# Kernel tuning notes

Measured on AMD Instinct MI355X. Metric: run time of the kernel, lower is better.

The kernel has to match this reference:

```python
import jax, jax.numpy as jnp
import numpy as np
import math

D_MODEL = 1024
N_HEAD = 16


def setup_inputs() -> dict:
    key = jax.random.key(0)
    k1, k2, k3 = jax.random.split(key, 3)
    B, S, E = 2, 2048, D_MODEL
    x = jax.random.normal(k1, (B, S, E), dtype=jnp.float32)
    # Linear weights stored as (in, out); init scaled like typical transformer init
    w_attn = jax.random.normal(k2, (E, 3 * E), dtype=jnp.float32) * (1.0 / math.sqrt(E))
    w_proj = jax.random.normal(k3, (E, E), dtype=jnp.float32) * (1.0 / math.sqrt(E))
    return {"x": x, "w_attn": w_attn, "w_proj": w_proj}


def reference(x, w_attn, w_proj):
    B, S, E = x.shape
    H = N_HEAD
    Dh = E // H
    qkv = x @ w_attn  # (B, S, 3E)
    q, k, v = jnp.split(qkv, 3, axis=-1)
    # (B, H, S, Dh)
    q = q.reshape(B, S, H, Dh).transpose(0, 2, 1, 3)
    k = k.reshape(B, S, H, Dh).transpose(0, 2, 1, 3)
    v = v.reshape(B, S, H, Dh).transpose(0, 2, 1, 3)
    scale = 1.0 / math.sqrt(Dh)
    att = jnp.einsum('bhqd,bhkd->bhqk', q, k) * scale  # (B, H, S, S)
    causal = jnp.tril(jnp.ones((S, S), dtype=bool))
    att = jnp.where(causal, att, -jnp.inf)
    att = jax.nn.softmax(att, axis=-1)
    # dropout = 0.0 (eval mode) -> identity
    y = jnp.einsum('bhqk,bhkd->bhqd', att, v)  # (B, H, S, Dh)
    y = y.transpose(0, 2, 1, 3).reshape(B, S, E)
    return y @ w_proj
```

## Files before the change

kernel.cpp:

```cpp
#include <hip/hip_runtime.h>
#include <hip/hip_bf16.h>

#define S_LEN 2048
#define EMB   1024
#define NH    16
#define DH    64
#define QKV_LD 3072

typedef __attribute__((ext_vector_type(8)))  __bf16 bf16x8;
typedef __attribute__((ext_vector_type(4)))  __bf16 bf16x4;
typedef __attribute__((ext_vector_type(4)))  float  f32x4;
typedef __attribute__((ext_vector_type(16))) float  f32x16;
typedef __attribute__((ext_vector_type(2)))  unsigned int u32x2;

__device__ __forceinline__ void gl_lds16(const void* g, void* l) {
  __builtin_amdgcn_global_load_lds(
      (const __attribute__((address_space(1))) void*)g,
      (__attribute__((address_space(3))) void*)l,
      16, 0, 0);
}

__global__ __launch_bounds__(256)
void prep_fused(const float* __restrict__ x, __bf16* __restrict__ xb,
                const float* __restrict__ w_attn, __bf16* __restrict__ wat,
                const float* __restrict__ w_proj, __bf16* __restrict__ wpt,
                int n8) {
  __shared__ float T[64][65];
  const int bid = blockIdx.x;
  const int tid = threadIdx.x;

  if (bid < 2048) {
    int i = bid * 256 + tid;
    if (i >= n8) return;
    const f32x4* p = (const f32x4*)(x + (size_t)i * 8);
    f32x4 a = p[0], b = p[1];
    bf16x8 o;
    #pragma unroll
    for (int j = 0; j < 4; j++) { o[j] = (__bf16)a[j]; o[4 + j] = (__bf16)b[j]; }
    *(bf16x8*)(xb + (size_t)i * 8) = o;
    return;
  }

  const float* W; __bf16* Wt; int K, N, k0, n0;
  if (bid < 2048 + 768) {
    int t = bid - 2048;
    W = w_attn; Wt = wat; K = 1024; N = 3072;
    n0 = (t % 48) * 64; k0 = (t / 48) * 64;
  } else {
    int t = bid - 2816;
    W = w_proj; Wt = wpt; K = 1024; N = 1024;
    n0 = (t & 15) * 64; k0 = (t >> 4) * 64;
  }
  #pragma unroll
  for (int t = 0; t < 16; t++) {
    int idx = tid + t * 256;
    int r = idx >> 6, c = idx & 63;
    T[r][c] = W[(size_t)(k0 + r) * N + n0 + c];
  }
  __syncthreads();
  #pragma unroll
  for (int t = 0; t < 16; t++) {
    int idx = tid + t * 256;
    int r = idx >> 6, c = idx & 63;
    Wt[(size_t)(n0 + r) * K + k0 + c] = (__bf16)T[c][r];
  }
}

#define TM 128
#define TK 32

template <typename OutT, int TNv>
__global__ __launch_bounds__(256, 2)
void gemm_bf16_mfma(const __bf16* __restrict__ A, const __bf16* __restrict__ Bt,
                    OutT* __restrict__ C, int M, int N, int K) {
  __shared__ __align__(16) __bf16 As[2][TM][TK];
  __shared__ __align__(16) __bf16 Bs[2][TNv][TK];
  const int tid  = threadIdx.x;
  const int lane = tid & 63;
  const int w    = tid >> 6;
  const int wr   = w >> 1, wc = w & 1;
  const int brow = blockIdx.y * TM;
  const int bcol = blockIdx.x * TNv;
  const int l15  = lane & 15;
  const int grp  = lane >> 4;

  constexpr int NBI = TNv / 64;
  constexpr int WCT = TNv / 2;
  constexpr int NN  = WCT / 16;

  auto stage = [&](int k0, int buf) {
    #pragma unroll
    for (int j = 0; j < 2; j++) {
      const int cid = w * 128 + j * 64 + lane;
      const int row = cid >> 2, k8 = (cid & 3) * 8;
      gl_lds16(A + (size_t)(brow + row) * K + k0 + k8,
               &As[buf][0][0] + (size_t)(w * 128 + j * 64) * 8);
    }
    #pragma unroll
    for (int j = 0; j < NBI; j++) {
      const int cid = (w * NBI + j) * 64 + lane;
      const int row = cid >> 2, k8 = (cid & 3) * 8;
      gl_lds16(Bt + (size_t)(bcol + row) * K + k0 + k8,
               &Bs[buf][0][0] + (size_t)((w * NBI + j) * 64) * 8);
    }
  };

  f32x4 acc[4][NN];
  #pragma unroll
  for (int m = 0; m < 4; m++)
    #pragma unroll
    for (int n = 0; n < NN; n++) acc[m][n] = (f32x4){0.f, 0.f, 0.f, 0.f};

  stage(0, 0);
  __syncthreads();

  const int nk = K / TK;
  for (int kt = 0; kt < nk; kt++) {
    const int cur = kt & 1;
    if (kt + 1 < nk) stage((kt + 1) * TK, cur ^ 1);

    bf16x8 a[4], b[NN];
    #pragma unroll
    for (int m = 0; m < 4; m++)
      a[m] = *(const bf16x8*)&As[cur][wr * 64 + m * 16 + l15][grp * 8];
    #pragma unroll
    for (int n = 0; n < NN; n++)
      b[n] = *(const bf16x8*)&Bs[cur][wc * WCT + n * 16 + l15][grp * 8];
    #pragma unroll
    for (int m = 0; m < 4; m++)
      #pragma unroll
      for (int n = 0; n < NN; n++)
        acc[m][n] = __builtin_amdgcn_mfma_f32_16x16x32_bf16(a[m], b[n], acc[m][n], 0, 0, 0);

    __syncthreads();
  }

  #pragma unroll
  for (int m = 0; m < 4; m++)
    #pragma unroll
    for (int r = 0; r < 4; r++) {
      const size_t row = (size_t)(brow + wr * 64 + m * 16 + grp * 4 + r);
      #pragma unroll
      for (int n = 0; n < NN; n++)
        C[row * N + bcol + wc * WCT + n * 16 + l15] = (OutT)acc[m][n][r];
    }
}

#define QB 64
#define KB 64
#define QSCALE 0.18033688f

__global__ __launch_bounds__(256, 4)
void attn_mfma(const __bf16* __restrict__ qkv, __bf16* __restrict__ y) {
  __shared__ __align__(16) __bf16 Ks[2][KB][64];
  __shared__ __align__(16) __bf16 Vs[2][4096];

  const int tid  = threadIdx.x;
  const int lane = tid & 63;
  const int w    = tid >> 6;

  const int bid = blockIdx.x;
  const int swz = (bid & 7) * 128 + (bid >> 3);
  const int g   = swz >> 5;
  const int i   = swz & 31;
  const int zig = (i & 1) ? (i >> 1) : 31 - (i >> 1);
  const int qtile = (g & 1) ? 31 - zig : zig;
  const int h = g & 15, b = g >> 4;

  const __bf16* base = qkv + (size_t)b * S_LEN * QKV_LD;

  const int l31 = lane & 31;
  const int hl  = lane >> 5;
  const int qh  = w >> 1;
  const int kh  = w & 1;

  const int voff32 = ((lane >> 4) & 1) * 2048 + hl * 128 + (lane & 15) * 8
                   + kh * 1024;

  auto stageK = [&](int j0, int buf) {
    #pragma unroll
    for (int j = 0; j < 2; j++) {
      const int cid = w * 128 + j * 64 + lane;
      const int r = cid >> 3, pc = cid & 7;
      const int lc = pc ^ (r & 7);
      gl_lds16(base + (size_t)(j0 + r) * QKV_LD + EMB + h * DH + lc * 8,
               (char*)&Ks[buf][0][0] + (w * 128 + j * 64) * 16);
    }
  };
  auto stageV = [&](int j0, int buf) {
    #pragma unroll
    for (int j = 0; j < 2; j++) {
      const int cid = w * 128 + j * 64 + lane;
      const int db = cid >> 7, sk = (cid >> 3) & 15;
      const int jr = (cid >> 1) & 3, ch = cid & 1;
      gl_lds16(base + (size_t)(j0 + sk * 4 + jr) * QKV_LD + 2 * EMB + h * DH
                    + db * 16 + ch * 8,
               (char*)&Vs[buf][0] + (w * 128 + j * 64) * 16);
    }
  };

  const int qbase = qtile * QB;
  const int ntiles = qtile + 1;
  const int q = qbase + qh * 32 + l31;

  bf16x8 qf[4];
  {
    const __bf16* qp = base + (size_t)q * QKV_LD + h * DH;
    #pragma unroll
    for (int dq = 0; dq < 4; dq++) {
      bf16x8 v = *(const bf16x8*)(qp + dq * 16 + hl * 8);
      #pragma unroll
      for (int i2 = 0; i2 < 8; i2++) qf[dq][i2] = (__bf16)((float)v[i2] * QSCALE);
    }
  }

  f32x16 o_acc[2];
  #pragma unroll
  for (int d2 = 0; d2 < 2; d2++)
    #pragma unroll
    for (int r = 0; r < 16; r++) o_acc[d2][r] = 0.f;
  float m = -1e30f, l = 0.f;

  auto process = [&](int cur, int j0, bool masked) {
    f32x16 s;
    #pragma unroll
    for (int r = 0; r < 16; r++) s[r] = 0.f;
    const int krow = kh * 32 + l31;
    __builtin_amdgcn_s_setprio(1);
    #pragma unroll
    for (int dq = 0; dq < 4; dq++) {
      bf16x8 kf = *(const bf16x8*)&Ks[cur][krow][((dq * 2 + hl) ^ (krow & 7)) * 8];
      s = __builtin_amdgcn_mfma_f32_32x32x16_bf16(kf, qf[dq], s, 0, 0, 0);
    }
    __builtin_amdgcn_s_setprio(0);

    if (masked) {
      const int lim = q - j0 - kh * 32 - 4 * hl;
      #pragma unroll
      for (int r = 0; r < 16; r++) {
        const int kl = (r & 3) + 8 * (r >> 2);
        if (kl > lim) s[r] = -2e30f;
      }
    }

    float tmax = s[0];
    #pragma unroll
    for (int r = 1; r < 16; r++) tmax = fmaxf(tmax, s[r]);
    tmax = fmaxf(tmax, __shfl_xor(tmax, 32));

    const bool grow = !__all(tmax <= m + 8.0f);
    float corr = 1.f;
    if (grow) {
      const float mnew = fmaxf(m, tmax);
      corr = __builtin_amdgcn_exp2f(m - mnew);
      m = mnew;
    }

    const unsigned vb =
        (unsigned)(uintptr_t)(__attribute__((address_space(3))) char*)(&Vs[cur][0])
        + (unsigned)voff32;
    u32x2 tv[8];
    asm volatile("ds_read_b64_tr_b16 %0, %1 offset:0"    : "=v"(tv[0]) : "v"(vb));
    asm volatile("ds_read_b64_tr_b16 %0, %1 offset:256"  : "=v"(tv[1]) : "v"(vb));
    asm volatile("ds_read_b64_tr_b16 %0, %1 offset:512"  : "=v"(tv[2]) : "v"(vb));
    asm volatile("ds_read_b64_tr_b16 %0, %1 offset:768"  : "=v"(tv[3]) : "v"(vb));
    asm volatile("ds_read_b64_tr_b16 %0, %1 offset:4096" : "=v"(tv[4]) : "v"(vb));
    asm volatile("ds_read_b64_tr_b16 %0, %1 offset:4352" : "=v"(tv[5]) : "v"(vb));
    asm volatile("ds_read_b64_tr_b16 %0, %1 offset:4608" : "=v"(tv[6]) : "v"(vb));
    asm volatile("ds_read_b64_tr_b16 %0, %1 offset:4864" : "=v"(tv[7]) : "v"(vb));

    float psum = 0.f;
    #pragma unroll
    for (int r = 0; r < 16; r++) {
      float p = __builtin_amdgcn_exp2f(s[r] - m);
      s[r] = p;
      psum += p;
    }

    bf16x8 pb0, pb1;
    #pragma unroll
    for (int i2 = 0; i2 < 8; i2++) {
      pb0[i2] = (__bf16)s[i2];
      pb1[i2] = (__bf16)s[8 + i2];
    }

    if (grow) {
      #pragma unroll
      for (int d2 = 0; d2 < 2; d2++)
        #pragma unroll
        for (int r = 0; r < 16; r++) o_acc[d2][r] *= corr;
    }

    asm volatile("s_waitcnt lgkmcnt(0)");
    __builtin_amdgcn_sched_barrier(0);
    __builtin_amdgcn_s_setprio(1);
    #pragma unroll
    for (int d2 = 0; d2 < 2; d2++) {
      bf16x8 a0, a1;
      ((u32x2*)&a0)[0] = tv[d2 * 4 + 0]; ((u32x2*)&a0)[1] = tv[d2 * 4 + 1];
      ((u32x2*)&a1)[0] = tv[d2 * 4 + 2]; ((u32x2*)&a1)[1] = tv[d2 * 4 + 3];
      o_acc[d2] = __builtin_amdgcn_mfma_f32_32x32x16_bf16(a0, pb0, o_acc[d2], 0, 0, 0);
      o_acc[d2] = __builtin_amdgcn_mfma_f32_32x32x16_bf16(a1, pb1, o_acc[d2], 0, 0, 0);
    }
    __builtin_amdgcn_s_setprio(0);

    psum += __shfl_xor(psum, 32);
    l = grow ? (l * corr + psum) : (l + psum);
  };

  stageK(0, 0);
  stageV(0, 0);
  __syncthreads();

  #pragma unroll 1
  for (int kt = 0; kt < ntiles - 1; kt++) {
    const int cur = kt & 1;
    stageK((kt + 1) * KB, cur ^ 1);
    stageV((kt + 1) * KB, cur ^ 1);
    process(cur, kt * KB, false);
    __syncthreads();
  }

  process((ntiles - 1) & 1, (ntiles - 1) * KB, true);

  __syncthreads();
  float* exO  = (float*)&Vs[0][0];
  float* exML = (float*)&Ks[0][0][0];
  const int slot = qh * 64 + lane;
  if (kh) {
    #pragma unroll
    for (int r = 0; r < 16; r++) {
      exO[r * 128 + slot]        = o_acc[0][r];
      exO[(16 + r) * 128 + slot] = o_acc[1][r];
    }
    exML[slot]       = m;
    exML[128 + slot] = l;
  }
  __syncthreads();
  if (!kh) {
    const float m1  = exML[slot];
    const float l1v = exML[128 + slot];
    const float mm = fmaxf(m, m1);
    const float c0 = __builtin_amdgcn_exp2f(m - mm);
    const float c1 = __builtin_amdgcn_exp2f(m1 - mm);
    const float inv = 1.f / (l * c0 + l1v * c1);
    __bf16* yrow = y + ((size_t)(b * S_LEN + q)) * EMB + h * DH;
    #pragma unroll
    for (int d2 = 0; d2 < 2; d2++)
      #pragma unroll
      for (int rq = 0; rq < 4; rq++) {
        bf16x4 o4;
        #pragma unroll
        for (int j = 0; j < 4; j++) {
          const int r = rq * 4 + j;
          float v = (o_acc[d2][r] * c0 + exO[(d2 * 16 + r) * 128 + slot] * c1) * inv;
          o4[j] = (__bf16)v;
        }
        *(bf16x4*)&yrow[d2 * 32 + rq * 8 + hl * 4] = o4;
      }
  }
}

extern "C" void kernel_launch(void* const* d_in, const int* in_sizes, int n_in,
                              void* d_out, int out_size, void* d_ws, size_t ws_size,
                              hipStream_t stream) {
  const float* x      = (const float*)d_in[0];
  const float* w_attn = (const float*)d_in[1];
  const float* w_proj = (const float*)d_in[2];
  float* out = (float*)d_out;

  const int B = in_sizes[0] / (S_LEN * EMB);
  const int M = B * S_LEN;

  __bf16* xb   = (__bf16*)d_ws;
  __bf16* wat  = xb  + (size_t)M * EMB;
  __bf16* wpt  = wat + (size_t)QKV_LD * EMB;
  __bf16* qkvb = wpt + (size_t)EMB * EMB;
  __bf16* yb   = qkvb + (size_t)M * QKV_LD;

  {
    int n8 = (M * EMB) / 8;
    prep_fused<<<dim3(3072), 256, 0, stream>>>(x, xb, w_attn, wat, w_proj, wpt, n8);
  }

  dim3 g1(QKV_LD / 128, M / TM);
  gemm_bf16_mfma<__bf16, 128><<<g1, 256, 0, stream>>>(xb, wat, qkvb, M, QKV_LD, EMB);

  attn_mfma<<<dim3(32 * NH * B), 256, 0, stream>>>(qkvb, yb);

  dim3 g3(EMB / 64, M / TM);
  gemm_bf16_mfma<float, 64><<<g3, 256, 0, stream>>>(yb, wpt, out, M, EMB, EMB);
}
```

Measured before the change: 109.2 us.

## Split long causal attention rows across two blocks with a merge kernel

Causal attention work is rebalanced so that query tiles 16-31, which have the most key tiles, are split into two halves along the key dimension, each handled by its own block. The halves write unnormalized partial outputs plus max/sum statistics into scratch memory, reusing the output buffer and the weight workspace. A new merge kernel combines them into the bf16 result. The goal is more uniform per-block work and better load balance across the XCDs, at the cost of an extra launch and extra fp32 scratch traffic; the occupancy hint is also raised from 4 to 5 blocks.

```diff
diff --git a/kernel.cpp b/kernel.cpp
--- a/kernel.cpp
+++ b/kernel.cpp
@@ -150,8 +150,9 @@
 #define KB 64
 #define QSCALE 0.18033688f
 
-__global__ __launch_bounds__(256, 4)
-void attn_mfma(const __bf16* __restrict__ qkv, __bf16* __restrict__ y) {
+__global__ __launch_bounds__(256, 5)
+void attn_mfma(const __bf16* __restrict__ qkv, __bf16* __restrict__ y,
+               float* __restrict__ pO, float* __restrict__ pml) {
   __shared__ __align__(16) __bf16 Ks[2][KB][64];
   __shared__ __align__(16) __bf16 Vs[2][4096];
 
@@ -160,12 +161,26 @@
   const int w    = tid >> 6;
 
   const int bid = blockIdx.x;
-  const int swz = (bid & 7) * 128 + (bid >> 3);
-  const int g   = swz >> 5;
-  const int i   = swz & 31;
-  const int zig = (i & 1) ? (i >> 1) : 31 - (i >> 1);
-  const int qtile = (g & 1) ? 31 - zig : zig;
+  const int xcd = bid & 7;
+  const int j   = bid >> 3;
+  const int g   = xcd * 4 + j / 48;
+  const int idx = j % 48;
+  const int t3  = idx / 3, r3 = idx - t3 * 3;
+
+  int qtile, it0, it1, khalf;
+  bool split, diag;
+  if (r3 == 2) {
+    qtile = 15 - t3; split = false; khalf = 0;
+    it0 = 0; it1 = qtile + 1; diag = true;
+  } else {
+    qtile = 31 - t3; split = true; khalf = r3;
+    const int half = (qtile + 2) >> 1;
+    it0 = khalf ? half : 0;
+    it1 = khalf ? qtile + 1 : half;
+    diag = (khalf == 1);
+  }
   const int h = g & 15, b = g >> 4;
+  const int pidx = split ? ((g * 16 + (qtile - 16)) * 2 + khalf) : 0;
 
   const __bf16* base = qkv + (size_t)b * S_LEN * QKV_LD;
 
@@ -179,28 +194,27 @@
 
   auto stageK = [&](int j0, int buf) {
     #pragma unroll
-    for (int j = 0; j < 2; j++) {
-      const int cid = w * 128 + j * 64 + lane;
+    for (int jj = 0; jj < 2; jj++) {
+      const int cid = w * 128 + jj * 64 + lane;
       const int r = cid >> 3, pc = cid & 7;
       const int lc = pc ^ (r & 7);
       gl_lds16(base + (size_t)(j0 + r) * QKV_LD + EMB + h * DH + lc * 8,
-               (char*)&Ks[buf][0][0] + (w * 128 + j * 64) * 16);
+               (char*)&Ks[buf][0][0] + (w * 128 + jj * 64) * 16);
     }
   };
   auto stageV = [&](int j0, int buf) {
     #pragma unroll
-    for (int j = 0; j < 2; j++) {
-      const int cid = w * 128 + j * 64 + lane;
+    for (int jj = 0; jj < 2; jj++) {
+      const int cid = w * 128 + jj * 64 + lane;
       const int db = cid >> 7, sk = (cid >> 3) & 15;
       const int jr = (cid >> 1) & 3, ch = cid & 1;
       gl_lds16(base + (size_t)(j0 + sk * 4 + jr) * QKV_LD + 2 * EMB + h * DH
                     + db * 16 + ch * 8,
-               (char*)&Vs[buf][0] + (w * 128 + j * 64) * 16);
+               (char*)&Vs[buf][0] + (w * 128 + jj * 64) * 16);
     }
   };
 
   const int qbase = qtile * QB;
-  const int ntiles = qtile + 1;
   const int q = qbase + qh * 32 + l31;
 
   bf16x8 qf[4];
@@ -308,20 +322,21 @@
     l = grow ? (l * corr + psum) : (l + psum);
   };
 
-  stageK(0, 0);
-  stageV(0, 0);
+  stageK(it0 * KB, 0);
+  stageV(it0 * KB, 0);
   __syncthreads();
 
+  const int nt = it1 - it0;
   #pragma unroll 1
-  for (int kt = 0; kt < ntiles - 1; kt++) {
-    const int cur = kt & 1;
-    stageK((kt + 1) * KB, cur ^ 1);
-    stageV((kt + 1) * KB, cur ^ 1);
-    process(cur, kt * KB, false);
+  for (int tt = 0; tt < nt - 1; tt++) {
+    const int cur = tt & 1;
+    stageK((it0 + tt + 1) * KB, cur ^ 1);
+    stageV((it0 + tt + 1) * KB, cur ^ 1);
+    process(cur, (it0 + tt) * KB, false);
     __syncthreads();
   }
 
-  process((ntiles - 1) & 1, (ntiles - 1) * KB, true);
+  process((nt - 1) & 1, (it1 - 1) * KB, diag);
 
   __syncthreads();
   float* exO  = (float*)&Vs[0][0];
@@ -343,21 +358,77 @@
     const float mm = fmaxf(m, m1);
     const float c0 = __builtin_amdgcn_exp2f(m - mm);
     const float c1 = __builtin_amdgcn_exp2f(m1 - mm);
-    const float inv = 1.f / (l * c0 + l1v * c1);
-    __bf16* yrow = y + ((size_t)(b * S_LEN + q)) * EMB + h * DH;
-    #pragma unroll
-    for (int d2 = 0; d2 < 2; d2++)
-      #pragma unroll
-      for (int rq = 0; rq < 4; rq++) {
-        bf16x4 o4;
+    const float lsum = l * c0 + l1v * c1;
+    if (split) {
+      float* prow = pO + (size_t)pidx * 4096 + (size_t)(qh * 32 + l31) * 64;
+      #pragma unroll
+      for (int d2 = 0; d2 < 2; d2++)
         #pragma unroll
-        for (int j = 0; j < 4; j++) {
-          const int r = rq * 4 + j;
-          float v = (o_acc[d2][r] * c0 + exO[(d2 * 16 + r) * 128 + slot] * c1) * inv;
-          o4[j] = (__bf16)v;
+        for (int rq = 0; rq < 4; rq++) {
+          f32x4 o4;
+          #pragma unroll
+          for (int jj = 0; jj < 4; jj++) {
+            const int r = rq * 4 + jj;
+            o4[jj] = o_acc[d2][r] * c0 + exO[(d2 * 16 + r) * 128 + slot] * c1;
+          }
+          *(f32x4*)&prow[d2 * 32 + rq * 8 + hl * 4] = o4;
         }
-        *(bf16x4*)&yrow[d2 * 32 + rq * 8 + hl * 4] = o4;
+      if (!hl) {
+        pml[(size_t)pidx * 128 + qh * 32 + l31]      = mm;
+        pml[(size_t)pidx * 128 + 64 + qh * 32 + l31] = lsum;
       }
+    } else {
+      const float inv = 1.f / lsum;
+      __bf16* yrow = y + ((size_t)(b * S_LEN + q)) * EMB + h * DH;
+      #pragma unroll
+      for (int d2 = 0; d2 < 2; d2++)
+        #pragma unroll
+        for (int rq = 0; rq < 4; rq++) {
+          bf16x4 o4;
+          #pragma unroll
+          for (int jj = 0; jj < 4; jj++) {
+            const int r = rq * 4 + jj;
+            float v = (o_acc[d2][r] * c0 + exO[(d2 * 16 + r) * 128 + slot] * c1) * inv;
+            o4[jj] = (__bf16)v;
+          }
+          *(bf16x4*)&yrow[d2 * 32 + rq * 8 + hl * 4] = o4;
+        }
+    }
+  }
+}
+
+__global__ __launch_bounds__(256)
+void attn_merge(const float* __restrict__ pO, const float* __restrict__ pml,
+                __bf16* __restrict__ y) {
+  const int mid = blockIdx.x;
+  const int g = mid >> 4, qrel = mid & 15;
+  const int qt = 16 + qrel;
+  const int b = g >> 4, h = g & 15;
+  const int p0 = (g * 16 + qrel) * 2, p1 = p0 + 1;
+  const int row = threadIdx.x >> 2;
+  const int d0  = (threadIdx.x & 3) * 16;
+
+  const float mA = pml[(size_t)p0 * 128 + row];
+  const float lA = pml[(size_t)p0 * 128 + 64 + row];
+  const float mB = pml[(size_t)p1 * 128 + row];
+  const float lB = pml[(size_t)p1 * 128 + 64 + row];
+  const float mm = fmaxf(mA, mB);
+  const float cA = __builtin_amdgcn_exp2f(mA - mm);
+  const float cB = __builtin_amdgcn_exp2f(mB - mm);
+  const float inv = 1.f / (lA * cA + lB * cB);
+
+  const float* OA = pO + (size_t)p0 * 4096 + (size_t)row * 64 + d0;
+  const float* OB = pO + (size_t)p1 * 4096 + (size_t)row * 64 + d0;
+  __bf16* yr = y + ((size_t)(b * S_LEN + qt * 64 + row)) * EMB + h * DH + d0;
+  #pragma unroll
+  for (int i = 0; i < 4; i++) {
+    f32x4 va = *(const f32x4*)(OA + i * 4);
+    f32x4 vb = *(const f32x4*)(OB + i * 4);
+    bf16x4 o;
+    #pragma unroll
+    for (int jj = 0; jj < 4; jj++)
+      o[jj] = (__bf16)((va[jj] * cA + vb[jj] * cB) * inv);
+    *(bf16x4*)(yr + i * 4) = o;
   }
 }
 
@@ -378,6 +449,9 @@
   __bf16* qkvb = wpt + (size_t)EMB * EMB;
   __bf16* yb   = qkvb + (size_t)M * QKV_LD;
 
+  float* pO  = out;
+  float* pml = (float*)wat;
+
   {
     int n8 = (M * EMB) / 8;
     prep_fused<<<dim3(3072), 256, 0, stream>>>(x, xb, w_attn, wat, w_proj, wpt, n8);
@@ -386,7 +460,8 @@
   dim3 g1(QKV_LD / 128, M / TM);
   gemm_bf16_mfma<__bf16, 128><<<g1, 256, 0, stream>>>(xb, wat, qkvb, M, QKV_LD, EMB);
 
-  attn_mfma<<<dim3(32 * NH * B), 256, 0, stream>>>(qkvb, yb);
+  attn_mfma<<<dim3(1536), 256, 0, stream>>>(qkvb, yb, pO, pml);
+  attn_merge<<<dim3(512), 256, 0, stream>>>(pO, pml, yb);
 
   dim3 g3(EMB / 64, M / TM);
   gemm_bf16_mfma<float, 64><<<g3, 256, 0, stream>>>(yb, wpt, out, M, EMB, EMB);
```

New measurement: 147.0 us. 34.6% more time.

## Use 128-key tiles with single-buffered LDS and in-iteration staged prefetch

Applied to the files above, without the earlier changes.

Doubles the key tile to 128 so each wave does two QK^T and four PV MFMAs per iteration, halving loop iterations and barrier overhead. Drops LDS double-buffering for a single 32KB buffer, and issues the next K and V loads mid-iteration once the current reads have drained, guarded by extra barriers. The last tile is always masked. Register pressure rises (two score blocks, 16 V fragments), and the single buffer exposes load latency at the top of each iteration.

```diff
diff --git a/kernel.cpp b/kernel.cpp
--- a/kernel.cpp
+++ b/kernel.cpp
@@ -147,13 +147,12 @@
 }
 
 #define QB 64
-#define KB 64
+#define KB 128
 #define QSCALE 0.18033688f
 
 __global__ __launch_bounds__(256, 4)
 void attn_mfma(const __bf16* __restrict__ qkv, __bf16* __restrict__ y) {
-  __shared__ __align__(16) __bf16 Ks[2][KB][64];
-  __shared__ __align__(16) __bf16 Vs[2][4096];
+  __shared__ __align__(16) char SMEM[33792];
 
   const int tid  = threadIdx.x;
   const int lane = tid & 63;
@@ -174,33 +173,33 @@
   const int qh  = w >> 1;
   const int kh  = w & 1;
 
-  const int voff32 = ((lane >> 4) & 1) * 2048 + hl * 128 + (lane & 15) * 8
-                   + kh * 1024;
-
-  auto stageK = [&](int j0, int buf) {
-    #pragma unroll
-    for (int j = 0; j < 2; j++) {
-      const int cid = w * 128 + j * 64 + lane;
+  const int voff32 = ((lane >> 4) & 1) * 2048 + hl * 128 + (lane & 15) * 8;
+
+  auto stageK = [&](int j0) {
+    #pragma unroll
+    for (int jj = 0; jj < 4; jj++) {
+      const int cid = w * 256 + jj * 64 + lane;
       const int r = cid >> 3, pc = cid & 7;
       const int lc = pc ^ (r & 7);
       gl_lds16(base + (size_t)(j0 + r) * QKV_LD + EMB + h * DH + lc * 8,
-               (char*)&Ks[buf][0][0] + (w * 128 + j * 64) * 16);
+               SMEM + cid * 16);
     }
   };
-  auto stageV = [&](int j0, int buf) {
-    #pragma unroll
-    for (int j = 0; j < 2; j++) {
-      const int cid = w * 128 + j * 64 + lane;
-      const int db = cid >> 7, sk = (cid >> 3) & 15;
-      const int jr = (cid >> 1) & 3, ch = cid & 1;
-      gl_lds16(base + (size_t)(j0 + sk * 4 + jr) * QKV_LD + 2 * EMB + h * DH
-                    + db * 16 + ch * 8,
-               (char*)&Vs[buf][0] + (w * 128 + j * 64) * 16);
+  auto stageV = [&](int j0) {
+    #pragma unroll
+    for (int jj = 0; jj < 4; jj++) {
+      const int cid = w * 256 + jj * 64 + lane;
+      const int c  = cid >> 9;
+      const int cc = cid & 511;
+      const int db = cc >> 7, sk = (cc >> 3) & 15;
+      const int jr = (cc >> 1) & 3, ch = cc & 1;
+      gl_lds16(base + (size_t)(j0 + c * 64 + sk * 4 + jr) * QKV_LD + 2 * EMB
+                    + h * DH + db * 16 + ch * 8,
+               SMEM + 16384 + cid * 16);
     }
   };
 
   const int qbase = qtile * QB;
-  const int ntiles = qtile + 1;
   const int q = qbase + qh * 32 + l31;
 
   bf16x8 qf[4];
@@ -221,31 +220,70 @@
     for (int r = 0; r < 16; r++) o_acc[d2][r] = 0.f;
   float m = -1e30f, l = 0.f;
 
-  auto process = [&](int cur, int j0, bool masked) {
-    f32x16 s;
-    #pragma unroll
-    for (int r = 0; r < 16; r++) s[r] = 0.f;
-    const int krow = kh * 32 + l31;
+  const int krow0 = kh * 64 + l31;
+  const int ksw   = l31 & 7;
+
+  auto iter = [&](int j0, bool masked, int jn, bool do_stage) {
+    asm volatile("s_waitcnt vmcnt(0)" ::: "memory");
+    __builtin_amdgcn_s_barrier();
+    __builtin_amdgcn_sched_barrier(0);
+
+    f32x16 s0, s1;
+    #pragma unroll
+    for (int r = 0; r < 16; r++) { s0[r] = 0.f; s1[r] = 0.f; }
     __builtin_amdgcn_s_setprio(1);
     #pragma unroll
     for (int dq = 0; dq < 4; dq++) {
-      bf16x8 kf = *(const bf16x8*)&Ks[cur][krow][((dq * 2 + hl) ^ (krow & 7)) * 8];
-      s = __builtin_amdgcn_mfma_f32_32x32x16_bf16(kf, qf[dq], s, 0, 0, 0);
+      const int col = ((dq * 2 + hl) ^ ksw) * 16;
+      bf16x8 kf0 = *(const bf16x8*)(SMEM + krow0 * 128 + col);
+      bf16x8 kf1 = *(const bf16x8*)(SMEM + (krow0 + 32) * 128 + col);
+      s0 = __builtin_amdgcn_mfma_f32_32x32x16_bf16(kf0, qf[dq], s0, 0, 0, 0);
+      s1 = __builtin_amdgcn_mfma_f32_32x32x16_bf16(kf1, qf[dq], s1, 0, 0, 0);
     }
     __builtin_amdgcn_s_setprio(0);
 
     if (masked) {
-      const int lim = q - j0 - kh * 32 - 4 * hl;
+      const int lim0 = q - j0 - kh * 64 - 4 * hl;
       #pragma unroll
       for (int r = 0; r < 16; r++) {
         const int kl = (r & 3) + 8 * (r >> 2);
-        if (kl > lim) s[r] = -2e30f;
+        if (kl > lim0)      s0[r] = -2e30f;
+        if (kl > lim0 - 32) s1[r] = -2e30f;
       }
     }
 
-    float tmax = s[0];
-    #pragma unroll
-    for (int r = 1; r < 16; r++) tmax = fmaxf(tmax, s[r]);
+    const unsigned vb =
+        (unsigned)(uintptr_t)(__attribute__((address_space(3))) char*)
+            (SMEM + 16384) + (unsigned)(kh * 8192 + voff32);
+    u32x2 tv0[8], tv1[8];
+    asm volatile("ds_read_b64_tr_b16 %0, %1 offset:0"    : "=v"(tv0[0]) : "v"(vb));
+    asm volatile("ds_read_b64_tr_b16 %0, %1 offset:256"  : "=v"(tv0[1]) : "v"(vb));
+    asm volatile("ds_read_b64_tr_b16 %0, %1 offset:512"  : "=v"(tv0[2]) : "v"(vb));
+    asm volatile("ds_read_b64_tr_b16 %0, %1 offset:768"  : "=v"(tv0[3]) : "v"(vb));
+    asm volatile("ds_read_b64_tr_b16 %0, %1 offset:4096" : "=v"(tv0[4]) : "v"(vb));
+    asm volatile("ds_read_b64_tr_b16 %0, %1 offset:4352" : "=v"(tv0[5]) : "v"(vb));
+    asm volatile("ds_read_b64_tr_b16 %0, %1 offset:4608" : "=v"(tv0[6]) : "v"(vb));
+    asm volatile("ds_read_b64_tr_b16 %0, %1 offset:4864" : "=v"(tv0[7]) : "v"(vb));
+    asm volatile("ds_read_b64_tr_b16 %0, %1 offset:1024" : "=v"(tv1[0]) : "v"(vb));
+    asm volatile("ds_read_b64_tr_b16 %0, %1 offset:1280" : "=v"(tv1[1]) : "v"(vb));
+    asm volatile("ds_read_b64_tr_b16 %0, %1 offset:1536" : "=v"(tv1[2]) : "v"(vb));
+    asm volatile("ds_read_b64_tr_b16 %0, %1 offset:1792" : "=v"(tv1[3]) : "v"(vb));
+    asm volatile("ds_read_b64_tr_b16 %0, %1 offset:5120" : "=v"(tv1[4]) : "v"(vb));
+    asm volatile("ds_read_b64_tr_b16 %0, %1 offset:5376" : "=v"(tv1[5]) : "v"(vb));
+    asm volatile("ds_read_b64_tr_b16 %0, %1 offset:5632" : "=v"(tv1[6]) : "v"(vb));
+    asm volatile("ds_read_b64_tr_b16 %0, %1 offset:5888" : "=v"(tv1[7]) : "v"(vb));
+
+    float x0 = fmaxf(fmaxf(s0[0], s1[0]),  fmaxf(s0[8],  s1[8]));
+    float x1 = fmaxf(fmaxf(s0[1], s1[1]),  fmaxf(s0[9],  s1[9]));
+    float x2 = fmaxf(fmaxf(s0[2], s1[2]),  fmaxf(s0[10], s1[10]));
+    float x3 = fmaxf(fmaxf(s0[3], s1[3]),  fmaxf(s0[11], s1[11]));
+    float x4 = fmaxf(fmaxf(s0[4], s1[4]),  fmaxf(s0[12], s1[12]));
+    float x5 = fmaxf(fmaxf(s0[5], s1[5]),  fmaxf(s0[13], s1[13]));
+    float x6 = fmaxf(fmaxf(s0[6], s1[6]),  fmaxf(s0[14], s1[14]));
+    float x7 = fmaxf(fmaxf(s0[7], s1[7]),  fmaxf(s0[15], s1[15]));
+    x0 = fmaxf(x0, x4); x1 = fmaxf(x1, x5);
+    x2 = fmaxf(x2, x6); x3 = fmaxf(x3, x7);
+    float tmax = fmaxf(fmaxf(x0, x2), fmaxf(x1, x3));
     tmax = fmaxf(tmax, __shfl_xor(tmax, 32));
 
     const bool grow = !__all(tmax <= m + 8.0f);
@@ -256,33 +294,41 @@
       m = mnew;
     }
 
-    const unsigned vb =
-        (unsigned)(uintptr_t)(__attribute__((address_space(3))) char*)(&Vs[cur][0])
-        + (unsigned)voff32;
-    u32x2 tv[8];
-    asm volatile("ds_read_b64_tr_b16 %0, %1 offset:0"    : "=v"(tv[0]) : "v"(vb));
-    asm volatile("ds_read_b64_tr_b16 %0, %1 offset:256"  : "=v"(tv[1]) : "v"(vb));
-    asm volatile("ds_read_b64_tr_b16 %0, %1 offset:512"  : "=v"(tv[2]) : "v"(vb));
-    asm volatile("ds_read_b64_tr_b16 %0, %1 offset:768"  : "=v"(tv[3]) : "v"(vb));
-    asm volatile("ds_read_b64_tr_b16 %0, %1 offset:4096" : "=v"(tv[4]) : "v"(vb));
-    asm volatile("ds_read_b64_tr_b16 %0, %1 offset:4352" : "=v"(tv[5]) : "v"(vb));
-    asm volatile("ds_read_b64_tr_b16 %0, %1 offset:4608" : "=v"(tv[6]) : "v"(vb));
-    asm volatile("ds_read_b64_tr_b16 %0, %1 offset:4864" : "=v"(tv[7]) : "v"(vb));
-
-    float psum = 0.f;
-    #pragma unroll
-    for (int r = 0; r < 16; r++) {
-      float p = __builtin_amdgcn_exp2f(s[r] - m);
-      s[r] = p;
-      psum += p;
-    }
-
-    bf16x8 pb0, pb1;
-    #pragma unroll
-    for (int i2 = 0; i2 < 8; i2++) {
-      pb0[i2] = (__bf16)s[i2];
-      pb1[i2] = (__bf16)s[8 + i2];
-    }
+    __builtin_amdgcn_s_barrier();
+    if (do_stage) stageK(jn);
+
+    asm volatile("s_waitcnt lgkmcnt(0)" ::: "memory");
+    __builtin_amdgcn_sched_barrier(0);
+    __builtin_amdgcn_s_barrier();
+    if (do_stage) stageV(jn);
+
+    float ps0 = 0.f, ps1 = 0.f, ps2 = 0.f, ps3 = 0.f;
+    bf16x8 pb00, pb01, pb10, pb11;
+    #pragma unroll
+    for (int r = 0; r < 16; r += 4) {
+      float p0 = __builtin_amdgcn_exp2f(s0[r]     - m);
+      float p1 = __builtin_amdgcn_exp2f(s0[r + 1] - m);
+      float p2 = __builtin_amdgcn_exp2f(s0[r + 2] - m);
+      float p3 = __builtin_amdgcn_exp2f(s0[r + 3] - m);
+      ps0 += p0; ps1 += p1; ps2 += p2; ps3 += p3;
+      if (r < 8) { pb00[r] = (__bf16)p0; pb00[r+1] = (__bf16)p1;
+                   pb00[r+2] = (__bf16)p2; pb00[r+3] = (__bf16)p3; }
+      else       { pb01[r-8] = (__bf16)p0; pb01[r-7] = (__bf16)p1;
+                   pb01[r-6] = (__bf16)p2; pb01[r-5] = (__bf16)p3; }
+    }
+    #pragma unroll
+    for (int r = 0; r < 16; r += 4) {
+      float p0 = __builtin_amdgcn_exp2f(s1[r]     - m);
+      float p1 = __builtin_amdgcn_exp2f(s1[r + 1] - m);
+      float p2 = __builtin_amdgcn_exp2f(s1[r + 2] - m);
+      float p3 = __builtin_amdgcn_exp2f(s1[r + 3] - m);
+      ps0 += p0; ps1 += p1; ps2 += p2; ps3 += p3;
+      if (r < 8) { pb10[r] = (__bf16)p0; pb10[r+1] = (__bf16)p1;
+                   pb10[r+2] = (__bf16)p2; pb10[r+3] = (__bf16)p3; }
+      else       { pb11[r-8] = (__bf16)p0; pb11[r-7] = (__bf16)p1;
+                   pb11[r-6] = (__bf16)p2; pb11[r-5] = (__bf16)p3; }
+    }
+    float psum = (ps0 + ps1) + (ps2 + ps3);
 
     if (grow) {
       #pragma unroll
@@ -291,16 +337,18 @@
         for (int r = 0; r < 16; r++) o_acc[d2][r] *= corr;
     }
 
-    asm volatile("s_waitcnt lgkmcnt(0)");
-    __builtin_amdgcn_sched_barrier(0);
     __builtin_amdgcn_s_setprio(1);
     #pragma unroll
     for (int d2 = 0; d2 < 2; d2++) {
-      bf16x8 a0, a1;
-      ((u32x2*)&a0)[0] = tv[d2 * 4 + 0]; ((u32x2*)&a0)[1] = tv[d2 * 4 + 1];
-      ((u32x2*)&a1)[0] = tv[d2 * 4 + 2]; ((u32x2*)&a1)[1] = tv[d2 * 4 + 3];
-      o_acc[d2] = __builtin_amdgcn_mfma_f32_32x32x16_bf16(a0, pb0, o_acc[d2], 0, 0, 0);
-      o_acc[d2] = __builtin_amdgcn_mfma_f32_32x32x16_bf16(a1, pb1, o_acc[d2], 0, 0, 0);
+      bf16x8 a0, a1, a2, a3;
+      ((u32x2*)&a0)[0] = tv0[d2 * 4 + 0]; ((u32x2*)&a0)[1] = tv0[d2 * 4 + 1];
+      ((u32x2*)&a1)[0] = tv0[d2 * 4 + 2]; ((u32x2*)&a1)[1] = tv0[d2 * 4 + 3];
+      ((u32x2*)&a2)[0] = tv1[d2 * 4 + 0]; ((u32x2*)&a2)[1] = tv1[d2 * 4 + 1];
+      ((u32x2*)&a3)[0] = tv1[d2 * 4 + 2]; ((u32x2*)&a3)[1] = tv1[d2 * 4 + 3];
+      o_acc[d2] = __builtin_amdgcn_mfma_f32_32x32x16_bf16(a0, pb00, o_acc[d2], 0, 0, 0);
+      o_acc[d2] = __builtin_amdgcn_mfma_f32_32x32x16_bf16(a1, pb01, o_acc[d2], 0, 0, 0);
+      o_acc[d2] = __builtin_amdgcn_mfma_f32_32x32x16_bf16(a2, pb10, o_acc[d2], 0, 0, 0);
+      o_acc[d2] = __builtin_amdgcn_mfma_f32_32x32x16_bf16(a3, pb11, o_acc[d2], 0, 0, 0);
     }
     __builtin_amdgcn_s_setprio(0);
 
@@ -308,24 +356,18 @@
     l = grow ? (l * corr + psum) : (l + psum);
   };
 
-  stageK(0, 0);
-  stageV(0, 0);
+  stageK(0);
+  stageV(0);
+
+  const int nt = (qtile + 2) >> 1;
+  #pragma unroll 1
+  for (int tt = 0; tt < nt; tt++) {
+    iter(tt * KB, tt == nt - 1, (tt + 1) * KB, tt + 1 < nt);
+  }
+
   __syncthreads();
-
-  #pragma unroll 1
-  for (int kt = 0; kt < ntiles - 1; kt++) {
-    const int cur = kt & 1;
-    stageK((kt + 1) * KB, cur ^ 1);
-    stageV((kt + 1) * KB, cur ^ 1);
-    process(cur, kt * KB, false);
-    __syncthreads();
-  }
-
-  process((ntiles - 1) & 1, (ntiles - 1) * KB, true);
-
-  __syncthreads();
-  float* exO  = (float*)&Vs[0][0];
-  float* exML = (float*)&Ks[0][0][0];
+  float* exO  = (float*)SMEM;
+  float* exML = (float*)(SMEM + 32768);
   const int slot = qh * 64 + lane;
   if (kh) {
     #pragma unroll
@@ -351,10 +393,10 @@
       for (int rq = 0; rq < 4; rq++) {
         bf16x4 o4;
         #pragma unroll
-        for (int j = 0; j < 4; j++) {
-          const int r = rq * 4 + j;
+        for (int jj = 0; jj < 4; jj++) {
+          const int r = rq * 4 + jj;
           float v = (o_acc[d2][r] * c0 + exO[(d2 * 16 + r) * 128 + slot] * c1) * inv;
-          o4[j] = (__bf16)v;
+          o4[jj] = (__bf16)v;
         }
         *(bf16x4*)&yrow[d2 * 32 + rq * 8 + hl * 4] = o4;
       }
```

Result: slower. 163.0 us (+49.3%).

## Widen attention tile to 128 queries with single-buffer in-loop staging

Applied to the files above, without the earlier changes.

The attention kernel now processes 128 query rows per block with 512 threads (8 waves), halving the grid and sharing each K/V tile across twice as many queries. Double-buffered LDS is replaced with a single buffer, and the next K and V tiles are issued inside the iteration after barriers, interleaved with the softmax math. The max and exp reductions are split into tree and multi-accumulator forms to shorten dependency chains. This cuts K/V global traffic and LDS footprint per query, but adds extra barriers per tile and a serialized two-phase epilogue, and fewer blocks may hurt load balance across the causal triangle.

```diff
diff --git a/kernel.cpp b/kernel.cpp
--- a/kernel.cpp
+++ b/kernel.cpp
@@ -146,25 +146,26 @@
     }
 }
 
-#define QB 64
+#define QB 128
 #define KB 64
 #define QSCALE 0.18033688f
 
-__global__ __launch_bounds__(256, 4)
+__global__ __launch_bounds__(512, 4)
 void attn_mfma(const __bf16* __restrict__ qkv, __bf16* __restrict__ y) {
-  __shared__ __align__(16) __bf16 Ks[2][KB][64];
-  __shared__ __align__(16) __bf16 Vs[2][4096];
+  __shared__ __align__(16) char SMEM[17408];
+  __bf16 (*Ks)[64] = (__bf16 (*)[64])SMEM;
+  __bf16* Vs = (__bf16*)(SMEM + 8192);
 
   const int tid  = threadIdx.x;
   const int lane = tid & 63;
   const int w    = tid >> 6;
 
   const int bid = blockIdx.x;
-  const int swz = (bid & 7) * 128 + (bid >> 3);
-  const int g   = swz >> 5;
-  const int i   = swz & 31;
-  const int zig = (i & 1) ? (i >> 1) : 31 - (i >> 1);
-  const int qtile = (g & 1) ? 31 - zig : zig;
+  const int swz = (bid & 7) * 64 + (bid >> 3);
+  const int g   = swz >> 4;
+  const int i   = swz & 15;
+  const int zig = (i & 1) ? (i >> 1) : 15 - (i >> 1);
+  const int qtile = (g & 1) ? 15 - zig : zig;
   const int h = g & 15, b = g >> 4;
 
   const __bf16* base = qkv + (size_t)b * S_LEN * QKV_LD;
@@ -177,31 +178,23 @@
   const int voff32 = ((lane >> 4) & 1) * 2048 + hl * 128 + (lane & 15) * 8
                    + kh * 1024;
 
-  auto stageK = [&](int j0, int buf) {
-    #pragma unroll
-    for (int j = 0; j < 2; j++) {
-      const int cid = w * 128 + j * 64 + lane;
-      const int r = cid >> 3, pc = cid & 7;
-      const int lc = pc ^ (r & 7);
-      gl_lds16(base + (size_t)(j0 + r) * QKV_LD + EMB + h * DH + lc * 8,
-               (char*)&Ks[buf][0][0] + (w * 128 + j * 64) * 16);
-    }
+  auto stageK = [&](int j0) {
+    const int cid = w * 64 + lane;
+    const int r = cid >> 3, pc = cid & 7;
+    const int lc = pc ^ (r & 7);
+    gl_lds16(base + (size_t)(j0 + r) * QKV_LD + EMB + h * DH + lc * 8,
+             SMEM + cid * 16);
   };
-  auto stageV = [&](int j0, int buf) {
-    #pragma unroll
-    for (int j = 0; j < 2; j++) {
-      const int cid = w * 128 + j * 64 + lane;
-      const int db = cid >> 7, sk = (cid >> 3) & 15;
-      const int jr = (cid >> 1) & 3, ch = cid & 1;
-      gl_lds16(base + (size_t)(j0 + sk * 4 + jr) * QKV_LD + 2 * EMB + h * DH
-                    + db * 16 + ch * 8,
-               (char*)&Vs[buf][0] + (w * 128 + j * 64) * 16);
-    }
+  auto stageV = [&](int j0) {
+    const int cid = w * 64 + lane;
+    const int db = cid >> 7, sk = (cid >> 3) & 15;
+    const int jr = (cid >> 1) & 3, ch = cid & 1;
+    gl_lds16(base + (size_t)(j0 + sk * 4 + jr) * QKV_LD + 2 * EMB + h * DH
+                  + db * 16 + ch * 8,
+             SMEM + 8192 + cid * 16);
   };
 
-  const int qbase = qtile * QB;
-  const int ntiles = qtile + 1;
-  const int q = qbase + qh * 32 + l31;
+  const int q = qtile * QB + qh * 32 + l31;
 
   bf16x8 qf[4];
   {
@@ -221,7 +214,11 @@
     for (int r = 0; r < 16; r++) o_acc[d2][r] = 0.f;
   float m = -1e30f, l = 0.f;
 
-  auto process = [&](int cur, int j0, bool masked) {
+  auto iter = [&](int j0, bool masked, int jn, bool do_stage) {
+    asm volatile("s_waitcnt vmcnt(0)" ::: "memory");
+    __builtin_amdgcn_s_barrier();
+    __builtin_amdgcn_sched_barrier(0);
+
     f32x16 s;
     #pragma unroll
     for (int r = 0; r < 16; r++) s[r] = 0.f;
@@ -229,7 +226,7 @@
     __builtin_amdgcn_s_setprio(1);
     #pragma unroll
     for (int dq = 0; dq < 4; dq++) {
-      bf16x8 kf = *(const bf16x8*)&Ks[cur][krow][((dq * 2 + hl) ^ (krow & 7)) * 8];
+      bf16x8 kf = *(const bf16x8*)&Ks[krow][((dq * 2 + hl) ^ (krow & 7)) * 8];
       s = __builtin_amdgcn_mfma_f32_32x32x16_bf16(kf, qf[dq], s, 0, 0, 0);
     }
     __builtin_amdgcn_s_setprio(0);
@@ -243,21 +240,8 @@
       }
     }
 
-    float tmax = s[0];
-    #pragma unroll
-    for (int r = 1; r < 16; r++) tmax = fmaxf(tmax, s[r]);
-    tmax = fmaxf(tmax, __shfl_xor(tmax, 32));
-
-    const bool grow = !__all(tmax <= m + 8.0f);
-    float corr = 1.f;
-    if (grow) {
-      const float mnew = fmaxf(m, tmax);
-      corr = __builtin_amdgcn_exp2f(m - mnew);
-      m = mnew;
-    }
-
     const unsigned vb =
-        (unsigned)(uintptr_t)(__attribute__((address_space(3))) char*)(&Vs[cur][0])
+        (unsigned)(uintptr_t)(__attribute__((address_space(3))) char*)(Vs)
         + (unsigned)voff32;
     u32x2 tv[8];
     asm volatile("ds_read_b64_tr_b16 %0, %1 offset:0"    : "=v"(tv[0]) : "v"(vb));
@@ -269,13 +253,43 @@
     asm volatile("ds_read_b64_tr_b16 %0, %1 offset:4608" : "=v"(tv[6]) : "v"(vb));
     asm volatile("ds_read_b64_tr_b16 %0, %1 offset:4864" : "=v"(tv[7]) : "v"(vb));
 
-    float psum = 0.f;
-    #pragma unroll
-    for (int r = 0; r < 16; r++) {
-      float p = __builtin_amdgcn_exp2f(s[r] - m);
-      s[r] = p;
-      psum += p;
-    }
+    float x0 = fmaxf(s[0], s[8]),  x1 = fmaxf(s[1], s[9]);
+    float x2 = fmaxf(s[2], s[10]), x3 = fmaxf(s[3], s[11]);
+    float x4 = fmaxf(s[4], s[12]), x5 = fmaxf(s[5], s[13]);
+    float x6 = fmaxf(s[6], s[14]), x7 = fmaxf(s[7], s[15]);
+    x0 = fmaxf(x0, x4); x1 = fmaxf(x1, x5);
+    x2 = fmaxf(x2, x6); x3 = fmaxf(x3, x7);
+    x0 = fmaxf(x0, x2); x1 = fmaxf(x1, x3);
+    float tmax = fmaxf(x0, x1);
+    tmax = fmaxf(tmax, __shfl_xor(tmax, 32));
+
+    const bool grow = !__all(tmax <= m + 8.0f);
+    float corr = 1.f;
+    if (grow) {
+      const float mnew = fmaxf(m, tmax);
+      corr = __builtin_amdgcn_exp2f(m - mnew);
+      m = mnew;
+    }
+
+    __builtin_amdgcn_s_barrier();
+    if (do_stage) stageK(jn);
+
+    asm volatile("s_waitcnt lgkmcnt(0)" ::: "memory");
+    __builtin_amdgcn_sched_barrier(0);
+    __builtin_amdgcn_s_barrier();
+    if (do_stage) stageV(jn);
+
+    float ps0 = 0.f, ps1 = 0.f, ps2 = 0.f, ps3 = 0.f;
+    #pragma unroll
+    for (int r = 0; r < 16; r += 4) {
+      float p0 = __builtin_amdgcn_exp2f(s[r]     - m);
+      float p1 = __builtin_amdgcn_exp2f(s[r + 1] - m);
+      float p2 = __builtin_amdgcn_exp2f(s[r + 2] - m);
+      float p3 = __builtin_amdgcn_exp2f(s[r + 3] - m);
+      s[r] = p0; s[r + 1] = p1; s[r + 2] = p2; s[r + 3] = p3;
+      ps0 += p0; ps1 += p1; ps2 += p2; ps3 += p3;
+    }
+    float psum = (ps0 + ps1) + (ps2 + ps3);
 
     bf16x8 pb0, pb1;
     #pragma unroll
@@ -291,8 +305,6 @@
         for (int r = 0; r < 16; r++) o_acc[d2][r] *= corr;
     }
 
-    asm volatile("s_waitcnt lgkmcnt(0)");
-    __builtin_amdgcn_sched_barrier(0);
     __builtin_amdgcn_s_setprio(1);
     #pragma unroll
     for (int d2 = 0; d2 < 2; d2++) {
@@ -308,56 +320,55 @@
     l = grow ? (l * corr + psum) : (l + psum);
   };
 
-  stageK(0, 0);
-  stageV(0, 0);
+  stageK(0);
+  stageV(0);
+
+  const int nt = 2 * qtile + 2;
+  #pragma unroll 1
+  for (int tt = 0; tt < nt; tt++) {
+    iter(tt * KB, tt >= nt - 2, (tt + 1) * KB, tt + 1 < nt);
+  }
+
   __syncthreads();
-
+  float* exO  = (float*)SMEM;
+  float* exML = (float*)(SMEM + 16384);
+  const int slot = (qh & 1) * 64 + lane;
   #pragma unroll 1
-  for (int kt = 0; kt < ntiles - 1; kt++) {
-    const int cur = kt & 1;
-    stageK((kt + 1) * KB, cur ^ 1);
-    stageV((kt + 1) * KB, cur ^ 1);
-    process(cur, kt * KB, false);
+  for (int ep = 0; ep < 2; ep++) {
+    const bool mine = (qh >> 1) == ep;
+    if (mine && kh) {
+      #pragma unroll
+      for (int r = 0; r < 16; r++) {
+        exO[r * 128 + slot]        = o_acc[0][r];
+        exO[(16 + r) * 128 + slot] = o_acc[1][r];
+      }
+      exML[slot]       = m;
+      exML[128 + slot] = l;
+    }
     __syncthreads();
-  }
-
-  process((ntiles - 1) & 1, (ntiles - 1) * KB, true);
-
-  __syncthreads();
-  float* exO  = (float*)&Vs[0][0];
-  float* exML = (float*)&Ks[0][0][0];
-  const int slot = qh * 64 + lane;
-  if (kh) {
-    #pragma unroll
-    for (int r = 0; r < 16; r++) {
-      exO[r * 128 + slot]        = o_acc[0][r];
-      exO[(16 + r) * 128 + slot] = o_acc[1][r];
-    }
-    exML[slot]       = m;
-    exML[128 + slot] = l;
-  }
-  __syncthreads();
-  if (!kh) {
-    const float m1  = exML[slot];
-    const float l1v = exML[128 + slot];
-    const float mm = fmaxf(m, m1);
-    const float c0 = __builtin_amdgcn_exp2f(m - mm);
-    const float c1 = __builtin_amdgcn_exp2f(m1 - mm);
-    const float inv = 1.f / (l * c0 + l1v * c1);
-    __bf16* yrow = y + ((size_t)(b * S_LEN + q)) * EMB + h * DH;
-    #pragma unroll
-    for (int d2 = 0; d2 < 2; d2++)
-      #pragma unroll
-      for (int rq = 0; rq < 4; rq++) {
-        bf16x4 o4;
+    if (mine && !kh) {
+      const float m1  = exML[slot];
+      const float l1v = exML[128 + slot];
+      const float mm = fmaxf(m, m1);
+      const float c0 = __builtin_amdgcn_exp2f(m - mm);
+      const float c1 = __builtin_amdgcn_exp2f(m1 - mm);
+      const float inv = 1.f / (l * c0 + l1v * c1);
+      __bf16* yrow = y + ((size_t)(b * S_LEN + q)) * EMB + h * DH;
+      #pragma unroll
+      for (int d2 = 0; d2 < 2; d2++)
         #pragma unroll
-        for (int j = 0; j < 4; j++) {
-          const int r = rq * 4 + j;
-          float v = (o_acc[d2][r] * c0 + exO[(d2 * 16 + r) * 128 + slot] * c1) * inv;
-          o4[j] = (__bf16)v;
+        for (int rq = 0; rq < 4; rq++) {
+          bf16x4 o4;
+          #pragma unroll
+          for (int jj = 0; jj < 4; jj++) {
+            const int r = rq * 4 + jj;
+            float v = (o_acc[d2][r] * c0 + exO[(d2 * 16 + r) * 128 + slot] * c1) * inv;
+            o4[jj] = (__bf16)v;
+          }
+          *(bf16x4*)&yrow[d2 * 32 + rq * 8 + hl * 4] = o4;
         }
-        *(bf16x4*)&yrow[d2 * 32 + rq * 8 + hl * 4] = o4;
-      }
+    }
+    __syncthreads();
   }
 }
 
@@ -386,7 +397,7 @@
   dim3 g1(QKV_LD / 128, M / TM);
   gemm_bf16_mfma<__bf16, 128><<<g1, 256, 0, stream>>>(xb, wat, qkvb, M, QKV_LD, EMB);
 
-  attn_mfma<<<dim3(32 * NH * B), 256, 0, stream>>>(qkvb, yb);
+  attn_mfma<<<dim3(512), 512, 0, stream>>>(qkvb, yb);
 
   dim3 g3(EMB / 64, M / TM);
   gemm_bf16_mfma<float, 64><<<g3, 256, 0, stream>>>(yb, wpt, out, M, EMB, EMB);
```

Result: slower. 115.6 us (+5.9%).
